# Optimization experiments

Hardware: AMD Instinct MI355X
Metric: run time of the kernel (lower is better)

The kernel has to match this reference:

```python
import jax, jax.numpy as jnp
import jax.lax as lax
import numpy as np

PS = 5           # patch_w for rgb (arch_opt.rgb=True)
PAD = PS // 2    # 2
WS = 29          # search window
SRAD = WS // 2   # 14
K = 14           # neigh_pad: number of nearest neighbors kept


def setup_inputs() -> dict:
    key = jax.random.key(0)
    k1, k2 = jax.random.split(key)
    noisy = jax.random.uniform(k1, (1, 3, 256, 256), jnp.float32) * 255.0
    sigma = jnp.array([25.0], jnp.float32)
    w_gray = jnp.array([0.2989, 0.587, 0.114], jnp.float32)  # fixed rgb2gray conv weight
    return {"noisy": noisy, "sigma": sigma, "w_gray": w_gray}


def reference(noisy, sigma, w_gray):
    t, c, h, w = noisy.shape
    # rescale to [-1,1] and remove per-image mean (as in forward)
    x = (noisy / 255.0 - 0.5) / 0.5
    means = x.mean((-2, -1), keepdims=True)
    x = x - means

    # grayscale search image (rgb2gray 1x1 conv)
    g = jnp.einsum('tchw,c->thw', x, w_gray)
    padT = PAD + SRAD  # 16: patch halo + search radius
    Gp = jnp.pad(g, ((0, 0), (padT, padT), (padT, padT)), mode='reflect')

    # --- patch-SSD over all ws*ws window offsets (KNN search) ---
    offs = jnp.arange(WS * WS)
    dys, dxs = offs // WS, offs % WS  # 0..28 <-> true offset -14..14
    Hc, Wc = h + 2 * PAD, w + 2 * PAD

    def crop(dy, dx):  # shifted crop covering all query patch supports
        return lax.dynamic_slice(Gp, (0, dy, dx), (t, Hc, Wc))

    S = jax.vmap(crop)(dys, dxs)                                   # [O,t,Hc,Wc]
    Cc = lax.dynamic_slice(Gp, (0, SRAD, SRAD), (t, Hc, Wc))       # center crop
    diff2 = (Cc[None] - S) ** 2                                    # [O,t,Hc,Wc]
    O = WS * WS
    kern = jnp.ones((1, 1, PS, PS), jnp.float32)
    d = lax.conv_general_dilated(diff2.reshape(O * t, 1, Hc, Wc), kern,
                                 (1, 1), 'VALID',
                                 dimension_numbers=('NCHW', 'OIHW', 'NCHW'))
    dists = d.reshape(O, t, h, w).transpose(1, 2, 3, 0)            # [t,h,w,O]

    negd, idx = lax.top_k(-dists, K)                               # k nearest offsets
    dists_k = -negd                                                # [t,h,w,K]

    # --- gather neighbor color patches ---
    Xp = jnp.pad(x, ((0, 0), (0, 0), (padT, padT), (padT, padT)), mode='reflect')
    patches = lax.conv_general_dilated_patches(Xp, (PS, PS), (1, 1), 'VALID')
    D = c * PS * PS
    Hg, Wg = h + 2 * SRAD, w + 2 * SRAD   # patch-center grid incl. search halo
    pf = patches.reshape(t, D, Hg * Wg)
    dy, dx = idx // WS, idx % WS          # 0..28; grid row = i + dy
    ii = jnp.arange(h)[None, :, None, None]
    jj = jnp.arange(w)[None, None, :, None]
    flat = ((ii + dy) * Wg + (jj + dx)).reshape(t, -1)             # [t, h*w*K]
    gathered = jax.vmap(lambda p, f: jnp.take(p, f, axis=1))(pf, flat)
    gathered = gathered.reshape(t, D, h * w, K)                    # [t,D,Q,K]

    # --- distance-softmax weighted patch aggregation ---
    sig = sigma[0] / 127.5  # noise std in rescaled units
    wts = jax.nn.softmax(-dists_k.reshape(t, h * w, K) / (sig * sig * PS * PS + 1e-8), axis=-1)
    pden = jnp.einsum('tdqk,tqk->tdq', gathered, wts).reshape(t, c, PS, PS, h, w)

    # --- fold (overlap-add) denoised patches + count normalization ---
    out = jnp.zeros((t, c, Hc, Wc), jnp.float32)
    cnt = jnp.zeros((1, 1, Hc, Wc), jnp.float32)
    for p in range(PS):
        for q in range(PS):
            out = out.at[:, :, p:p + h, q:q + w].add(pden[:, :, p, q])
            cnt = cnt.at[:, :, p:p + h, q:q + w].add(1.0)
    deno = out[:, :, PAD:-PAD, PAD:-PAD] / cnt[:, :, PAD:-PAD, PAD:-PAD]

    deno = deno + means
    deno = 255.0 * (deno * 0.5 + 0.5)
    return deno
```

## Files before the change

kernel.cpp:

```cpp
#include <hip/hip_runtime.h>

#define EXT 40
#define SQ (EXT*EXT)

__device__ __forceinline__ unsigned um_min(unsigned a, unsigned b){ return a < b ? a : b; }
__device__ __forceinline__ unsigned um_max(unsigned a, unsigned b){ return a > b ? a : b; }
__device__ __forceinline__ unsigned med3u(unsigned a, unsigned b, unsigned c){
  unsigned d;
  asm("v_med3_u32 %0, %1, %2, %3" : "=v"(d) : "v"(a), "v"(b), "v"(c));
  return d;
}

__device__ __forceinline__ void insert14(unsigned (&a)[14], unsigned key){
  unsigned kp  = um_min(key, a[0]);
  unsigned n0  = um_max(a[1], kp);
  unsigned n13 = um_min(a[13], kp);
  unsigned nn[12];
  #pragma unroll
  for (int i = 1; i <= 12; ++i) nn[i-1] = med3u(a[i], a[i+1], kp);
  a[0] = n0;
  #pragma unroll
  for (int i = 1; i <= 12; ++i) a[i] = nn[i-1];
  a[13] = n13;
}

__global__ void k_prep(const float* __restrict__ noisy, float* __restrict__ Xp,
                       float* __restrict__ accG){
  int idx = blockIdx.x * 256 + threadIdx.x;
  if (idx < 3*260*260) accG[idx] = 0.f;
  if (idx >= 288*288) return;
  int P = idx / 288, Q = idx - P*288;
  int sy = P - 16; sy = sy < 0 ? -sy : sy; sy = sy > 255 ? 510 - sy : sy;
  int sx = Q - 16; sx = sx < 0 ? -sx : sx; sx = sx > 255 ? 510 - sx : sx;
  const float inv = 1.0f / 127.5f;
  int src = sy*256 + sx;
  #pragma unroll
  for (int c = 0; c < 3; ++c)
    Xp[c*82944 + idx] = noisy[c*65536 + src] * inv - 1.0f;
}

template<int DX>
__device__ __forceinline__ void ssd_step(const float* rowbase, unsigned obase,
                                         const float (&cp)[5][5], float cpsq,
                                         float (&win)[5][5], float (&ring)[5],
                                         float& winsq, unsigned (&arr)[14]){
  constexpr int nc = (DX + 4) % 5;
  #pragma unroll
  for (int u = 0; u < 5; ++u) win[u][nc] = rowbase[u*EXT + DX + 4];
  float nssq = win[0][nc]*win[0][nc];
  #pragma unroll
  for (int u = 1; u < 5; ++u) nssq = fmaf(win[u][nc], win[u][nc], nssq);
  winsq += (nssq - ring[nc]);
  ring[nc] = nssq;
  float c0=0.f, c1=0.f, c2=0.f, c3=0.f, c4=0.f;
  #pragma unroll
  for (int v = 0; v < 5; ++v){
    constexpr int dummy = 0; (void)dummy;
    c0 = fmaf(cp[0][v], win[0][(DX + v) % 5], c0);
    c1 = fmaf(cp[1][v], win[1][(DX + v) % 5], c1);
    c2 = fmaf(cp[2][v], win[2][(DX + v) % 5], c2);
    c3 = fmaf(cp[3][v], win[3][(DX + v) % 5], c3);
    c4 = fmaf(cp[4][v], win[4][(DX + v) % 5], c4);
  }
  float cross = ((c0 + c1) + (c2 + c3)) + c4;
  float dist = fmaf(cross, -2.0f, cpsq + winsq);
  dist = fmaxf(dist, 0.0f);
  insert14(arr, (__float_as_uint(dist) & 0xFFFFFC00u) | (obase + (unsigned)DX));
}

template<int DX>
__device__ __forceinline__ void row_steps(const float* rowbase, unsigned obase,
                                          const float (&cp)[5][5], float cpsq,
                                          float (&win)[5][5], float (&ring)[5],
                                          float& winsq, unsigned (&arr)[14]){
  if constexpr (DX < 29){
    ssd_step<DX>(rowbase, obase, cp, cpsq, win, ring, winsq, arr);
    row_steps<DX+1>(rowbase, obase, cp, cpsq, win, ring, winsq, arr);
  }
}

__global__ __launch_bounds__(256, 4) void k_search(const float* __restrict__ Xp,
      const float* __restrict__ sigma, const float* __restrict__ wgray,
      float* __restrict__ accG){
  __shared__ float sXp[3*SQ];
  __shared__ float sG[SQ];
  __shared__ unsigned sCand[3*64*14];
  __shared__ float sWsum[64];
  __shared__ float sFold[12*12*3];

  const int tid = threadIdx.x;
  const int w = tid >> 6, l = tid & 63;
  const int ly = l >> 3, lx = l & 7;
  const int bi = blockIdx.y * 8, bj = blockIdx.x * 8;

  for (int t = tid; t < 3*SQ; t += 256){
    int c = t / SQ; int r2 = t - c*SQ; int rr = r2 / EXT; int cc = r2 - rr*EXT;
    sXp[t] = Xp[c*82944 + (bi+rr)*288 + (bj+cc)];
  }
  if (tid < 64) sWsum[tid] = 0.f;
  for (int t = tid; t < 432; t += 256) sFold[t] = 0.f;
  __syncthreads();
  const float w0 = wgray[0], w1 = wgray[1], w2 = wgray[2];
  for (int t = tid; t < SQ; t += 256)
    sG[t] = w0*sXp[t] + w1*sXp[SQ+t] + w2*sXp[2*SQ+t];
  __syncthreads();

  float cp[5][5];
  #pragma unroll
  for (int u = 0; u < 5; ++u)
    #pragma unroll
    for (int v = 0; v < 5; ++v)
      cp[u][v] = sG[(14 + ly + u)*EXT + 14 + lx + v];
  float cpsq = 0.f;
  #pragma unroll
  for (int v = 0; v < 5; ++v){
    float cs = cp[0][v]*cp[0][v];
    #pragma unroll
    for (int u = 1; u < 5; ++u) cs = fmaf(cp[u][v], cp[u][v], cs);
    cpsq += cs;
  }

  unsigned arr[14];
  #pragma unroll
  for (int k = 0; k < 14; ++k) arr[k] = 0xFFFFFFFFu;

  const int dy0 = (w == 0) ? 0 : 1 + 7*w;
  const int dy1 = dy0 + ((w == 0) ? 8 : 7);

  #pragma unroll 1
  for (int dy = dy0; dy < dy1; ++dy){
    const float* rowbase = &sG[(dy + ly)*EXT + lx];
    float win[5][5], ring[5], winsq;
    #pragma unroll
    for (int v = 0; v < 4; ++v){
      #pragma unroll
      for (int u = 0; u < 5; ++u) win[u][v] = rowbase[u*EXT + v];
      float cs = win[0][v]*win[0][v];
      #pragma unroll
      for (int u = 1; u < 5; ++u) cs = fmaf(win[u][v], win[u][v], cs);
      ring[v] = cs;
    }
    ring[4] = 0.f;
    winsq = (ring[0] + ring[1]) + (ring[2] + ring[3]);
    row_steps<0>(rowbase, (unsigned)(dy*29), cp, cpsq, win, ring, winsq, arr);
  }

  if (w){
    #pragma unroll
    for (int k = 0; k < 14; ++k) sCand[((w-1)*64 + l)*14 + k] = arr[k];
  }
  __syncthreads();
  if (!w){
    for (int q = 0; q < 3; ++q)
      #pragma unroll
      for (int k = 0; k < 14; ++k)
        insert14(arr, sCand[(q*64 + l)*14 + k]);
    #pragma unroll
    for (int k = 0; k < 14; ++k) sCand[l*14 + k] = arr[k];
  }
  __syncthreads();

  float sg = sigma[0] * (1.0f / 127.5f);
  const float invT = 1.0f / (sg*sg*25.0f + 1e-8f);
  const float dmin = __uint_as_float(sCand[l*14 + 13] & 0xFFFFFC00u);

  float wgt[4]; int ndy[4], ndx[4];
  const int nk = (w < 2) ? 4 : 3;
  float Sp = 0.f;
  #pragma unroll
  for (int m = 0; m < 4; ++m){
    if (m < nk){
      unsigned kk = sCand[l*14 + (w + 4*m)];
      float d = __uint_as_float(kk & 0xFFFFFC00u);
      int o = (int)(kk & 0x3FFu);
      wgt[m] = expf(-(d - dmin) * invT);
      ndy[m] = o / 29; ndx[m] = o - ndy[m]*29;
      Sp += wgt[m];
    }
  }
  atomicAdd(&sWsum[l], Sp);
  __syncthreads();
  const float invS = 1.0f / sWsum[l];
  #pragma unroll
  for (int m = 0; m < 4; ++m) if (m < nk) wgt[m] *= invS;

  #pragma unroll
  for (int c = 0; c < 3; ++c){
    float acc[5][5];
    #pragma unroll
    for (int u = 0; u < 5; ++u)
      #pragma unroll
      for (int v = 0; v < 5; ++v) acc[u][v] = 0.f;
    #pragma unroll
    for (int m = 0; m < 4; ++m){
      if (m < nk){
        const float* pb = &sXp[c*SQ + (ly + ndy[m])*EXT + lx + ndx[m]];
        float g = wgt[m];
        #pragma unroll
        for (int u = 0; u < 5; ++u)
          #pragma unroll
          for (int v = 0; v < 5; ++v)
            acc[u][v] = fmaf(g, pb[u*EXT + v], acc[u][v]);
      }
    }
    #pragma unroll
    for (int u = 0; u < 5; ++u)
      #pragma unroll
      for (int v = 0; v < 5; ++v)
        atomicAdd(&sFold[((ly+u)*12 + (lx+v))*3 + c], acc[u][v]);
  }
  __syncthreads();
  for (int t = tid; t < 432; t += 256){
    int c = t % 3; int rc = t / 3; int rr = rc / 12; int cc = rc - rr*12;
    atomicAdd(&accG[c*67600 + (bi+rr)*260 + (bj+cc)], sFold[t]);
  }
}

__global__ void k_finish(const float* __restrict__ accG, float* __restrict__ out){
  int idx = blockIdx.x * 256 + threadIdx.x;
  if (idx >= 3*65536) return;
  int c = idx >> 16; int rem = idx & 65535; int y = rem >> 8; int x = rem & 255;
  int cy = min(4, y + 2) - max(0, y - 253) + 1;
  int cx = min(4, x + 2) - max(0, x - 253) + 1;
  float v = accG[c*67600 + (y+2)*260 + (x+2)] / (float)(cy * cx);
  out[idx] = 127.5f * v + 127.5f;
}

extern "C" void kernel_launch(void* const* d_in, const int* in_sizes, int n_in,
                              void* d_out, int out_size, void* d_ws, size_t ws_size,
                              hipStream_t stream) {
  const float* noisy = (const float*)d_in[0];
  const float* sigma = (const float*)d_in[1];
  const float* wgray = (const float*)d_in[2];
  float* out  = (float*)d_out;
  float* Xp   = (float*)d_ws;
  float* accG = Xp + 3*288*288;

  k_prep<<<dim3(793), dim3(256), 0, stream>>>(noisy, Xp, accG);
  k_search<<<dim3(32, 32), dim3(256), 0, stream>>>(Xp, sigma, wgray, accG);
  k_finish<<<dim3(768), dim3(256), 0, stream>>>(accG, out);
}
```

Baseline: 232.5 us.

## Split offset search across eight waves with tree merge of top-k lists

Each block now runs 512 threads, so the 29 search rows are split across eight waves of 3-4 rows instead of four waves of 7-8, shortening the serial SSD/insert loop per thread. The per-wave top-14 lists are combined by a three-level tree reduction in shared memory rather than serially in one wave. The color tile buffer now shares storage with the candidate buffer and is loaded after the search, which lowers LDS use. The costs are extra barriers, a bigger launch bound that may cap registers per thread, and a color tile reload from global memory placed on the critical path.

Measured after the change: 829.0 us. 3.57x slower.

```diff
diff --git a/kernel.cpp b/kernel.cpp
--- a/kernel.cpp
+++ b/kernel.cpp
@@ -55,7 +55,6 @@
   float c0=0.f, c1=0.f, c2=0.f, c3=0.f, c4=0.f;
   #pragma unroll
   for (int v = 0; v < 5; ++v){
-    constexpr int dummy = 0; (void)dummy;
     c0 = fmaf(cp[0][v], win[0][(DX + v) % 5], c0);
     c1 = fmaf(cp[1][v], win[1][(DX + v) % 5], c1);
     c2 = fmaf(cp[2][v], win[2][(DX + v) % 5], c2);
@@ -79,30 +78,30 @@
   }
 }
 
-__global__ __launch_bounds__(256, 4) void k_search(const float* __restrict__ Xp,
+__global__ __launch_bounds__(512, 8) void k_search(const float* __restrict__ Xp,
       const float* __restrict__ sigma, const float* __restrict__ wgray,
       float* __restrict__ accG){
-  __shared__ float sXp[3*SQ];
   __shared__ float sG[SQ];
-  __shared__ unsigned sCand[3*64*14];
+  __shared__ float uni[3*SQ];
   __shared__ float sWsum[64];
   __shared__ float sFold[12*12*3];
+
+  unsigned* sCand = (unsigned*)uni;
+  float*    sXp   = uni;
 
   const int tid = threadIdx.x;
   const int w = tid >> 6, l = tid & 63;
   const int ly = l >> 3, lx = l & 7;
   const int bi = blockIdx.y * 8, bj = blockIdx.x * 8;
 
-  for (int t = tid; t < 3*SQ; t += 256){
-    int c = t / SQ; int r2 = t - c*SQ; int rr = r2 / EXT; int cc = r2 - rr*EXT;
-    sXp[t] = Xp[c*82944 + (bi+rr)*288 + (bj+cc)];
-  }
   if (tid < 64) sWsum[tid] = 0.f;
-  for (int t = tid; t < 432; t += 256) sFold[t] = 0.f;
-  __syncthreads();
+  if (tid < 432) sFold[tid] = 0.f;
   const float w0 = wgray[0], w1 = wgray[1], w2 = wgray[2];
-  for (int t = tid; t < SQ; t += 256)
-    sG[t] = w0*sXp[t] + w1*sXp[SQ+t] + w2*sXp[2*SQ+t];
+  for (int t = tid; t < SQ; t += 512){
+    int rr = t / EXT, cc = t - rr*EXT;
+    int base = (bi+rr)*288 + (bj+cc);
+    sG[t] = w0*Xp[base] + w1*Xp[82944 + base] + w2*Xp[2*82944 + base];
+  }
   __syncthreads();
 
   float cp[5][5];
@@ -124,11 +123,12 @@
   #pragma unroll
   for (int k = 0; k < 14; ++k) arr[k] = 0xFFFFFFFFu;
 
-  const int dy0 = (w == 0) ? 0 : 1 + 7*w;
-  const int dy1 = dy0 + ((w == 0) ? 8 : 7);
+  const int dy0 = (w < 5) ? w*4 : 20 + (w-5)*3;
+  const int nrows = (w < 5) ? 4 : 3;
 
   #pragma unroll 1
-  for (int dy = dy0; dy < dy1; ++dy){
+  for (int r = 0; r < nrows; ++r){
+    const int dy = dy0 + r;
     const float* rowbase = &sG[(dy + ly)*EXT + lx];
     float win[5][5], ring[5], winsq;
     #pragma unroll
@@ -145,16 +145,34 @@
     row_steps<0>(rowbase, (unsigned)(dy*29), cp, cpsq, win, ring, winsq, arr);
   }
 
-  if (w){
-    #pragma unroll
-    for (int k = 0; k < 14; ++k) sCand[((w-1)*64 + l)*14 + k] = arr[k];
-  }
-  __syncthreads();
-  if (!w){
-    for (int q = 0; q < 3; ++q)
-      #pragma unroll
-      for (int k = 0; k < 14; ++k)
-        insert14(arr, sCand[(q*64 + l)*14 + k]);
+  if (w >= 4){
+    #pragma unroll
+    for (int k = 0; k < 14; ++k) sCand[(w-4)*896 + l*14 + k] = arr[k];
+  }
+  __syncthreads();
+  if (w < 4){
+    #pragma unroll
+    for (int k = 0; k < 14; ++k) insert14(arr, sCand[w*896 + l*14 + k]);
+  }
+  __syncthreads();
+  if (w == 2 || w == 3){
+    #pragma unroll
+    for (int k = 0; k < 14; ++k) sCand[(w-2)*896 + l*14 + k] = arr[k];
+  }
+  __syncthreads();
+  if (w < 2){
+    #pragma unroll
+    for (int k = 0; k < 14; ++k) insert14(arr, sCand[w*896 + l*14 + k]);
+  }
+  __syncthreads();
+  if (w == 1){
+    #pragma unroll
+    for (int k = 0; k < 14; ++k) sCand[l*14 + k] = arr[k];
+  }
+  __syncthreads();
+  if (w == 0){
+    #pragma unroll
+    for (int k = 0; k < 14; ++k) insert14(arr, sCand[l*14 + k]);
     #pragma unroll
     for (int k = 0; k < 14; ++k) sCand[l*14 + k] = arr[k];
   }
@@ -164,13 +182,13 @@
   const float invT = 1.0f / (sg*sg*25.0f + 1e-8f);
   const float dmin = __uint_as_float(sCand[l*14 + 13] & 0xFFFFFC00u);
 
-  float wgt[4]; int ndy[4], ndx[4];
-  const int nk = (w < 2) ? 4 : 3;
+  const int nk = (w < 6) ? 2 : 1;
+  float wgt[2]; int ndy[2], ndx[2];
   float Sp = 0.f;
   #pragma unroll
-  for (int m = 0; m < 4; ++m){
+  for (int m = 0; m < 2; ++m){
     if (m < nk){
-      unsigned kk = sCand[l*14 + (w + 4*m)];
+      unsigned kk = sCand[l*14 + (m ? w + 8 : w)];
       float d = __uint_as_float(kk & 0xFFFFFC00u);
       int o = (int)(kk & 0x3FFu);
       wgt[m] = expf(-(d - dmin) * invT);
@@ -182,7 +200,13 @@
   __syncthreads();
   const float invS = 1.0f / sWsum[l];
   #pragma unroll
-  for (int m = 0; m < 4; ++m) if (m < nk) wgt[m] *= invS;
+  for (int m = 0; m < 2; ++m) if (m < nk) wgt[m] *= invS;
+
+  for (int t = tid; t < 3*SQ; t += 512){
+    int c = t / SQ; int r2 = t - c*SQ; int rr = r2 / EXT; int cc = r2 - rr*EXT;
+    sXp[t] = Xp[c*82944 + (bi+rr)*288 + (bj+cc)];
+  }
+  __syncthreads();
 
   #pragma unroll
   for (int c = 0; c < 3; ++c){
@@ -192,7 +216,7 @@
       #pragma unroll
       for (int v = 0; v < 5; ++v) acc[u][v] = 0.f;
     #pragma unroll
-    for (int m = 0; m < 4; ++m){
+    for (int m = 0; m < 2; ++m){
       if (m < nk){
         const float* pb = &sXp[c*SQ + (ly + ndy[m])*EXT + lx + ndx[m]];
         float g = wgt[m];
@@ -210,7 +234,7 @@
         atomicAdd(&sFold[((ly+u)*12 + (lx+v))*3 + c], acc[u][v]);
   }
   __syncthreads();
-  for (int t = tid; t < 432; t += 256){
+  for (int t = tid; t < 432; t += 512){
     int c = t % 3; int rc = t / 3; int rr = rc / 12; int cc = rc - rr*12;
     atomicAdd(&accG[c*67600 + (bi+rr)*260 + (bj+cc)], sFold[t]);
   }
@@ -237,6 +261,6 @@
   float* accG = Xp + 3*288*288;
 
   k_prep<<<dim3(793), dim3(256), 0, stream>>>(noisy, Xp, accG);
-  k_search<<<dim3(32, 32), dim3(256), 0, stream>>>(Xp, sigma, wgray, accG);
+  k_search<<<dim3(32, 32), dim3(512), 0, stream>>>(Xp, sigma, wgray, accG);
   k_finish<<<dim3(768), dim3(256), 0, stream>>>(accG, out);
 }
```

## Software-pipeline SSD window loads two columns ahead with 8-slot ring buffer

Applied to the files above, without the earlier changes.

The inner SSD sweep now keeps an 8-column register ring and issues LDS loads for column DX+6 while computing step DX, so shared-memory latency overlaps with the FMA and insertion work. The running window sum of squares is recomputed from per-column values rather than updated incrementally. Launch bounds drop from 4 to 2 blocks per CU to give the larger register window room, and the per-wave row split is rearranged. This trades occupancy for more instruction-level parallelism inside each thread.

Result: no change. 234.7 us (+1.0%).

```diff
diff --git a/kernel.cpp b/kernel.cpp
--- a/kernel.cpp
+++ b/kernel.cpp
@@ -39,28 +39,33 @@
     Xp[c*82944 + idx] = noisy[c*65536 + src] * inv - 1.0f;
 }
 
+template<int COL>
+__device__ __forceinline__ void load_col(const float* rowbase, float (&win)[5][8]){
+  #pragma unroll
+  for (int u = 0; u < 5; ++u) win[u][COL & 7] = rowbase[u*EXT + COL];
+}
+
 template<int DX>
-__device__ __forceinline__ void ssd_step(const float* rowbase, unsigned obase,
-                                         const float (&cp)[5][5], float cpsq,
-                                         float (&win)[5][5], float (&ring)[5],
-                                         float& winsq, unsigned (&arr)[14]){
-  constexpr int nc = (DX + 4) % 5;
-  #pragma unroll
-  for (int u = 0; u < 5; ++u) win[u][nc] = rowbase[u*EXT + DX + 4];
-  float nssq = win[0][nc]*win[0][nc];
-  #pragma unroll
-  for (int u = 1; u < 5; ++u) nssq = fmaf(win[u][nc], win[u][nc], nssq);
-  winsq += (nssq - ring[nc]);
-  ring[nc] = nssq;
-  float c0=0.f, c1=0.f, c2=0.f, c3=0.f, c4=0.f;
-  #pragma unroll
-  for (int v = 0; v < 5; ++v){
-    constexpr int dummy = 0; (void)dummy;
-    c0 = fmaf(cp[0][v], win[0][(DX + v) % 5], c0);
-    c1 = fmaf(cp[1][v], win[1][(DX + v) % 5], c1);
-    c2 = fmaf(cp[2][v], win[2][(DX + v) % 5], c2);
-    c3 = fmaf(cp[3][v], win[3][(DX + v) % 5], c3);
-    c4 = fmaf(cp[4][v], win[4][(DX + v) % 5], c4);
+__device__ __forceinline__ void math_step(unsigned obase, const float (&cp)[5][5],
+    float cpsq, const float (&win)[5][8], float (&ssq)[8], unsigned (&arr)[14]){
+  constexpr int s4 = (DX + 4) & 7;
+  float ns = win[0][s4]*win[0][s4];
+  #pragma unroll
+  for (int u = 1; u < 5; ++u) ns = fmaf(win[u][s4], win[u][s4], ns);
+  ssq[s4] = ns;
+  float winsq = ((ssq[DX&7] + ssq[(DX+1)&7]) + (ssq[(DX+2)&7] + ssq[(DX+3)&7])) + ns;
+  float c0 = cp[0][0]*win[0][DX&7];
+  float c1 = cp[1][0]*win[1][DX&7];
+  float c2 = cp[2][0]*win[2][DX&7];
+  float c3 = cp[3][0]*win[3][DX&7];
+  float c4 = cp[4][0]*win[4][DX&7];
+  #pragma unroll
+  for (int v = 1; v < 5; ++v){
+    c0 = fmaf(cp[0][v], win[0][(DX+v)&7], c0);
+    c1 = fmaf(cp[1][v], win[1][(DX+v)&7], c1);
+    c2 = fmaf(cp[2][v], win[2][(DX+v)&7], c2);
+    c3 = fmaf(cp[3][v], win[3][(DX+v)&7], c3);
+    c4 = fmaf(cp[4][v], win[4][(DX+v)&7], c4);
   }
   float cross = ((c0 + c1) + (c2 + c3)) + c4;
   float dist = fmaf(cross, -2.0f, cpsq + winsq);
@@ -69,17 +74,17 @@
 }
 
 template<int DX>
-__device__ __forceinline__ void row_steps(const float* rowbase, unsigned obase,
-                                          const float (&cp)[5][5], float cpsq,
-                                          float (&win)[5][5], float (&ring)[5],
-                                          float& winsq, unsigned (&arr)[14]){
+__device__ __forceinline__ void pipe_steps(const float* rowbase, unsigned obase,
+    const float (&cp)[5][5], float cpsq, float (&win)[5][8], float (&ssq)[8],
+    unsigned (&arr)[14]){
   if constexpr (DX < 29){
-    ssd_step<DX>(rowbase, obase, cp, cpsq, win, ring, winsq, arr);
-    row_steps<DX+1>(rowbase, obase, cp, cpsq, win, ring, winsq, arr);
-  }
-}
-
-__global__ __launch_bounds__(256, 4) void k_search(const float* __restrict__ Xp,
+    if constexpr (DX + 6 <= 32) load_col<DX+6>(rowbase, win);
+    math_step<DX>(obase, cp, cpsq, win, ssq, arr);
+    pipe_steps<DX+1>(rowbase, obase, cp, cpsq, win, ssq, arr);
+  }
+}
+
+__global__ __launch_bounds__(256, 2) void k_search(const float* __restrict__ Xp,
       const float* __restrict__ sigma, const float* __restrict__ wgray,
       float* __restrict__ accG){
   __shared__ float sXp[3*SQ];
@@ -124,25 +129,25 @@
   #pragma unroll
   for (int k = 0; k < 14; ++k) arr[k] = 0xFFFFFFFFu;
 
-  const int dy0 = (w == 0) ? 0 : 1 + 7*w;
-  const int dy1 = dy0 + ((w == 0) ? 8 : 7);
+  const int dy0 = (w == 0) ? 0 : (w == 1 ? 7 : (w == 2 ? 15 : 22));
+  const int nrows = (w == 1) ? 8 : 7;
 
   #pragma unroll 1
-  for (int dy = dy0; dy < dy1; ++dy){
+  for (int r = 0; r < nrows; ++r){
+    const int dy = dy0 + r;
     const float* rowbase = &sG[(dy + ly)*EXT + lx];
-    float win[5][5], ring[5], winsq;
+    float win[5][8], ssq[8];
+    load_col<0>(rowbase, win); load_col<1>(rowbase, win);
+    load_col<2>(rowbase, win); load_col<3>(rowbase, win);
+    load_col<4>(rowbase, win); load_col<5>(rowbase, win);
     #pragma unroll
     for (int v = 0; v < 4; ++v){
-      #pragma unroll
-      for (int u = 0; u < 5; ++u) win[u][v] = rowbase[u*EXT + v];
       float cs = win[0][v]*win[0][v];
       #pragma unroll
       for (int u = 1; u < 5; ++u) cs = fmaf(win[u][v], win[u][v], cs);
-      ring[v] = cs;
+      ssq[v] = cs;
     }
-    ring[4] = 0.f;
-    winsq = (ring[0] + ring[1]) + (ring[2] + ring[3]);
-    row_steps<0>(rowbase, (unsigned)(dy*29), cp, cpsq, win, ring, winsq, arr);
+    pipe_steps<0>(rowbase, (unsigned)(dy*29), cp, cpsq, win, ssq, arr);
   }
 
   if (w){
```
